# Performance work log

Measured on AMD Instinct MI355X. Metric: run time of the kernel, lower is better.

The kernel has to match this reference:

```python
import jax, jax.numpy as jnp
import numpy as np

B = 16        # batch
N = 1024      # satellite nodes
D = 256       # hidden size
H = 8         # attention heads
NUM_LAYERS = 3          # config.n_layer_aa
L = NUM_LAYERS + 1      # distinct GAT layers
EPS = 1e-5


def setup_inputs() -> dict:
    key = jax.random.key(0)
    ks = jax.random.split(key, 6)
    graph_vectors = jax.random.normal(ks[0], (B, N + 1, D), dtype=jnp.float32)
    graph = jax.random.uniform(ks[1], (B, N, N), dtype=jnp.float32)
    scale = 0.02
    Wq = jax.random.normal(ks[2], (L, D, D), dtype=jnp.float32) * scale
    Wk = jax.random.normal(ks[3], (L, D, D), dtype=jnp.float32) * scale
    Wv = jax.random.normal(ks[4], (L, D, D), dtype=jnp.float32) * scale
    Wo = jax.random.normal(ks[5], (L, D, D), dtype=jnp.float32) * scale
    ln_g = jnp.ones((L, D), dtype=jnp.float32)
    ln_b = jnp.zeros((L, D), dtype=jnp.float32)
    return {"graph_vectors": graph_vectors, "graph": graph,
            "Wq": Wq, "Wk": Wk, "Wv": Wv, "Wo": Wo,
            "ln_g": ln_g, "ln_b": ln_b}


def _layer_norm(x, g, b):
    mu = jnp.mean(x, axis=-1, keepdims=True)
    var = jnp.var(x, axis=-1, keepdims=True)
    return (x - mu) * jax.lax.rsqrt(var + EPS) * g + b


def _gat(x_q, x_kv, wq, wk, wv, wo, g, b):
    # multi-head attention: x_q [B,Lq,D] attends over x_kv [B,Lk,D]
    Bq, Lq, _ = x_q.shape
    Lk = x_kv.shape[1]
    dh = D // H
    q = (x_q @ wq).reshape(Bq, Lq, H, dh)
    k = (x_kv @ wk).reshape(Bq, Lk, H, dh)
    v = (x_kv @ wv).reshape(Bq, Lk, H, dh)
    scores = jnp.einsum('bqhd,bkhd->bhqk', q, k) / jnp.sqrt(jnp.float32(dh))
    attn = jax.nn.softmax(scores, axis=-1)
    o = jnp.einsum('bhqk,bkhd->bqhd', attn, v).reshape(Bq, Lq, D)
    out = o @ wo
    return _layer_norm(out + x_q, g, b)


def reference(graph_vectors, graph, Wq, Wk, Wv, Wo, ln_g, ln_b):
    relay = graph_vectors[:, :1, :]        # [B,1,D]
    sat = graph_vectors[:, 1:, :]          # [B,N,D]
    # layer 0: relay attends over satellites
    relay = _gat(relay, sat, Wq[0], Wk[0], Wv[0], Wo[0], ln_g[0], ln_b[0])
    # satellite = (satellite^T @ graph)^T -> [B,N,D]
    sat = jnp.einsum('bnd,bnm->bmd', sat, graph)
    gv = jnp.concatenate([relay, sat], axis=1)   # [B,N+1,D]
    # middle layers: full self-attention over all N+1 nodes
    for i in range(1, NUM_LAYERS):
        gv = _gat(gv, gv, Wq[i], Wk[i], Wv[i], Wo[i], ln_g[i], ln_b[i])
    relay_u = gv[:, :1, :]
    sat_u = gv[:, 1:, :]
    z = _gat(relay_u, sat_u, Wq[-1], Wk[-1], Wv[-1], Wo[-1], ln_g[-1], ln_b[-1])[:, 0, :]
    return z, sat_u
```

## Files before the change

kernel.cpp:

```cpp
#include <hip/hip_runtime.h>
#include <hip/hip_bf16.h>
#include <math.h>

#define BD   256
#define NH   8
#define DH   32
#define NB   16
#define NN   1024
#define LQ   1025
#define EPSV 1e-5f
#define KP   1088

typedef unsigned short ushort_t;
typedef __attribute__((ext_vector_type(8))) short short8;
typedef __attribute__((ext_vector_type(4))) float f32x4;

static __device__ __forceinline__ ushort_t f2b(float x) {
  union { __hip_bfloat16 h; ushort_t u; } cv;
  cv.h = __float2bfloat16(x);
  return cv.u;
}
static __device__ __forceinline__ float b2f(ushort_t u) {
  union { float f; unsigned v; } c; c.v = ((unsigned)u) << 16; return c.f;
}
static __device__ __forceinline__ float fexp2(float x) {
#if defined(__has_builtin)
#if __has_builtin(__builtin_amdgcn_exp2f)
  return __builtin_amdgcn_exp2f(x);
#else
  return exp2f(x);
#endif
#else
  return exp2f(x);
#endif
}

__global__ void k_copy_cast(const float* __restrict__ in, float* __restrict__ X,
                            ushort_t* __restrict__ Xh, long n) {
  long stride = (long)gridDim.x * 256;
  for (long i = (long)blockIdx.x * 256 + threadIdx.x; i < n; i += stride) {
    float v = in[i];
    X[i] = v;
    Xh[i] = f2b(v);
  }
}

__global__ void k_sat_out(const float* __restrict__ X, float* __restrict__ out) {
  long n = (long)NB * NN * BD;
  long stride = (long)gridDim.x * 256;
  for (long i = (long)blockIdx.x * 256 + threadIdx.x; i < n; i += stride) {
    long b = i / ((long)NN * BD);
    long r = i - b * ((long)NN * BD);
    out[i] = X[b * (long)LQ * BD + BD + r];
  }
}

__global__ __launch_bounds__(256) void k_wtrans(const float* __restrict__ Wq,
                                                const float* __restrict__ Wk,
                                                const float* __restrict__ Wv,
                                                const float* __restrict__ Wo,
                                                ushort_t* __restrict__ Wt) {
  const float C1 = 0.17677669529663687f * 1.4426950408889634f;
  int mat = blockIdx.y;
  int type = mat >> 2, layer = mat & 3;
  const float* src = (type == 0) ? Wq : (type == 1) ? Wk : (type == 2) ? Wv : Wo;
  src += (long)layer * BD * BD;
  float scv = (type == 0) ? C1 : 1.f;
  ushort_t* dst = Wt + (long)mat * BD * BD;
  __shared__ float t[32][33];
  int k0 = (blockIdx.x & 7) * 32, n0 = (blockIdx.x >> 3) * 32;
  int tid = threadIdx.x;
  for (int i = tid; i < 1024; i += 256) {
    int kk = i >> 5, nn = i & 31;
    t[kk][nn] = src[(long)(k0 + kk) * BD + n0 + nn];
  }
  __syncthreads();
  for (int i = tid; i < 1024; i += 256) {
    int nn = i >> 5, kk = i & 31;
    dst[(long)(n0 + nn) * BD + k0 + kk] = f2b(t[kk][nn] * scv);
  }
}

__global__ __launch_bounds__(256) void k_gtrans(const float* __restrict__ G,
                                                ushort_t* __restrict__ Ght) {
  __shared__ ushort_t t[64][65];
  int b = blockIdx.y;
  int m0 = (blockIdx.x & 15) * 64, n0 = (blockIdx.x >> 4) * 64;
  const float* Gb = G + (long)b * NN * NN;
  ushort_t* dst = Ght + (long)b * NN * NN;
  int tid = threadIdx.x;
  #pragma unroll
  for (int rr = 0; rr < 16; rr++) {
    int n = rr * 4 + (tid >> 6);
    int m = tid & 63;
    t[m][n] = f2b(Gb[(long)(n0 + n) * NN + m0 + m]);
  }
  __syncthreads();
  #pragma unroll
  for (int rr = 0; rr < 8; rr++) {
    int m = rr * 8 + (tid >> 5);
    int n2 = (tid & 31) * 2;
    unsigned w = (unsigned)t[m][n2] | ((unsigned)t[m][n2 + 1] << 16);
    *(unsigned*)&dst[(long)(m0 + m) * NN + n0 + n2] = w;
  }
}

__global__ __launch_bounds__(256) void k_satT(const ushort_t* __restrict__ Xh,
                                              ushort_t* __restrict__ satT) {
  __shared__ ushort_t t[64][65];
  int b = blockIdx.y;
  int n0 = (blockIdx.x & 15) * 64, d0 = (blockIdx.x >> 4) * 64;
  const ushort_t* src = Xh + ((long)b * LQ + 1) * BD;
  ushort_t* dst = satT + (long)b * BD * NN;
  int tid = threadIdx.x;
  #pragma unroll
  for (int rr = 0; rr < 16; rr++) {
    int n = rr * 4 + (tid >> 6);
    int d = tid & 63;
    t[n][d] = src[(long)(n0 + n) * BD + d0 + d];
  }
  __syncthreads();
  #pragma unroll
  for (int rr = 0; rr < 8; rr++) {
    int d = rr * 8 + (tid >> 5);
    int n2 = (tid & 31) * 2;
    unsigned w = (unsigned)t[n2][d] | ((unsigned)t[n2 + 1][d] << 16);
    *(unsigned*)&dst[(long)(d0 + d) * NN + n0 + n2] = w;
  }
}

__global__ __launch_bounds__(256) void k_vtrans(const ushort_t* __restrict__ Vh,
                                                ushort_t* __restrict__ VhT) {
  __shared__ ushort_t t[64][65];
  int b = blockIdx.z;
  int n0 = blockIdx.x * 64, d0 = blockIdx.y * 64;
  const ushort_t* src = Vh + (long)b * LQ * BD;
  ushort_t* dst = VhT + (long)b * BD * KP;
  int tid = threadIdx.x;
  #pragma unroll
  for (int rr = 0; rr < 16; rr++) {
    int n = rr * 4 + (tid >> 6);
    int d = tid & 63;
    int key = n0 + n;
    t[n][d] = (key < LQ) ? src[(long)key * BD + d0 + d] : (ushort_t)0;
  }
  __syncthreads();
  #pragma unroll
  for (int rr = 0; rr < 8; rr++) {
    int d = rr * 8 + (tid >> 5);
    int n2 = (tid & 31) * 2;
    unsigned w = (unsigned)t[n2][d] | ((unsigned)t[n2 + 1][d] << 16);
    *(unsigned*)&dst[(long)(d0 + d) * KP + n0 + n2] = w;
  }
}

static __device__ __forceinline__ void gemm_core(const ushort_t* __restrict__ A,
                                                 const ushort_t* __restrict__ W,
                                                 ushort_t* Ws,
                                                 float* __restrict__ Cf,
                                                 ushort_t* __restrict__ Ch,
                                                 int M, int m0, int n0) {
  int tid = threadIdx.x;
  int wave = tid >> 6, lane = tid & 63;
  int l15 = lane & 15, quad = lane >> 4;
  for (int i = tid; i < 64 * 32; i += 256) {
    int r = i >> 5, c8 = (i & 31) * 8;
    *(uint4*)&Ws[r * 264 + c8] = *(const uint4*)&W[(long)(n0 + r) * 256 + c8];
  }
  __syncthreads();
  int mrow = m0 + wave * 16 + l15;
  if (mrow > M - 1) mrow = M - 1;
  f32x4 acc[4];
  #pragma unroll
  for (int f = 0; f < 4; f++) { acc[f][0] = 0.f; acc[f][1] = 0.f; acc[f][2] = 0.f; acc[f][3] = 0.f; }
  #pragma unroll
  for (int k0 = 0; k0 < 256; k0 += 32) {
    short8 a = *(const short8*)&A[(long)mrow * 256 + k0 + quad * 8];
    #pragma unroll
    for (int f = 0; f < 4; f++) {
      short8 bb = *(const short8*)&Ws[(f * 16 + l15) * 264 + k0 + quad * 8];
      acc[f] = __builtin_amdgcn_mfma_f32_16x16x32_bf16(a, bb, acc[f], 0, 0, 0);
    }
  }
  #pragma unroll
  for (int f = 0; f < 4; f++)
    #pragma unroll
    for (int r = 0; r < 4; r++) {
      int m = m0 + wave * 16 + quad * 4 + r;
      if (m < M) {
        long idx = (long)m * 256 + n0 + f * 16 + l15;
        if (Cf) Cf[idx] = acc[f][r];
        else    Ch[idx] = f2b(acc[f][r]);
      }
    }
}

__global__ __launch_bounds__(256) void gemm_qkv(const ushort_t* __restrict__ Xh,
                                                const ushort_t* __restrict__ Wt, int layer,
                                                ushort_t* __restrict__ Qo,
                                                ushort_t* __restrict__ Ko,
                                                ushort_t* __restrict__ Vo, int M) {
  __shared__ __align__(16) ushort_t As[128 * 72];
  __shared__ __align__(16) ushort_t Bs[128 * 72];
  int tid = threadIdx.x;
  int wave = tid >> 6, lane = tid & 63;
  int l15 = lane & 15, quad = lane >> 4;
  int wr = wave >> 1, wc = wave & 1;
  int which = blockIdx.y >> 1;
  int n0 = (blockIdx.y & 1) * 128;
  const ushort_t* W = Wt + (long)(which * 4 + layer) * 65536;
  ushort_t* C = (which == 0) ? Qo : (which == 1) ? Ko : Vo;
  int m0 = blockIdx.x * 128;

  int sr = tid >> 2, sc = (tid & 3) * 8;
  int ar0 = m0 + sr;      if (ar0 > M - 1) ar0 = M - 1;
  int ar1 = m0 + sr + 64; if (ar1 > M - 1) ar1 = M - 1;
  const ushort_t* aSrc0 = Xh + (long)ar0 * 256 + sc;
  const ushort_t* aSrc1 = Xh + (long)ar1 * 256 + sc;
  const ushort_t* bSrc0 = W + (long)(n0 + sr) * 256 + sc;
  const ushort_t* bSrc1 = bSrc0 + 64 * 256;
  ushort_t* aDst0 = &As[sr * 72 + sc];
  ushort_t* aDst1 = aDst0 + 64 * 72;
  ushort_t* bDst0 = &Bs[sr * 72 + sc];
  ushort_t* bDst1 = bDst0 + 64 * 72;

  {
    uint4 a0 = *(const uint4*)aSrc0;
    uint4 a1 = *(const uint4*)aSrc1;
    uint4 b0 = *(const uint4*)bSrc0;
    uint4 b1 = *(const uint4*)bSrc1;
    *(uint4*)aDst0 = a0; *(uint4*)aDst1 = a1;
    *(uint4*)bDst0 = b0; *(uint4*)bDst1 = b1;
  }
  __syncthreads();

  f32x4 acc[4][4];
  #pragma unroll
  for (int i = 0; i < 4; i++)
    #pragma unroll
    for (int j = 0; j < 4; j++) { acc[i][j][0] = 0.f; acc[i][j][1] = 0.f; acc[i][j][2] = 0.f; acc[i][j][3] = 0.f; }

  for (int ks = 0; ks < 8; ks++) {
    bool more = (ks < 7);
    uint4 na0, na1, nb0, nb1;
    if (more) {
      aSrc0 += 32; aSrc1 += 32; bSrc0 += 32; bSrc1 += 32;
      na0 = *(const uint4*)aSrc0;
      na1 = *(const uint4*)aSrc1;
      nb0 = *(const uint4*)bSrc0;
      nb1 = *(const uint4*)bSrc1;
    }
    short8 af[4], bf[4];
    #pragma unroll
    for (int f = 0; f < 4; f++)
      af[f] = *(const short8*)&As[(wr * 64 + f * 16 + l15) * 72 + quad * 8];
    #pragma unroll
    for (int f = 0; f < 4; f++)
      bf[f] = *(const short8*)&Bs[(wc * 64 + f * 16 + l15) * 72 + quad * 8];
    #pragma unroll
    for (int i = 0; i < 4; i++)
      #pragma unroll
      for (int j = 0; j < 4; j++)
        acc[i][j] = __builtin_amdgcn_mfma_f32_16x16x32_bf16(af[i], bf[j], acc[i][j], 0, 0, 0);
    if (more) {
      __syncthreads();
      *(uint4*)aDst0 = na0;
      *(uint4*)aDst1 = na1;
      *(uint4*)bDst0 = nb0;
      *(uint4*)bDst1 = nb1;
      __syncthreads();
    }
  }

  #pragma unroll
  for (int i = 0; i < 4; i++)
    #pragma unroll
    for (int j = 0; j < 4; j++)
      #pragma unroll
      for (int r = 0; r < 4; r++) {
        int m = m0 + wr * 64 + i * 16 + quad * 4 + r;
        if (m < M) {
          int n = n0 + wc * 64 + j * 16 + l15;
          C[(long)m * 256 + n] = f2b(acc[i][j][r]);
        }
      }
}

__global__ __launch_bounds__(256) void gemm_kv(const ushort_t* __restrict__ Xh,
                                               const ushort_t* __restrict__ Wt, int layer,
                                               ushort_t* __restrict__ Ko,
                                               ushort_t* __restrict__ Vo) {
  __shared__ __align__(16) ushort_t Ws[64 * 264];
  int which = blockIdx.y >> 2, n0 = (blockIdx.y & 3) * 64;
  int b = blockIdx.z;
  const ushort_t* W = Wt + (long)((which + 1) * 4 + layer) * 65536;
  const ushort_t* A = Xh + (long)b * (LQ * BD) + BD;
  ushort_t* C = ((which == 0) ? Ko : Vo) + (long)b * (NN * BD);
  gemm_core(A, W, Ws, nullptr, C, NN, blockIdx.x * 64, n0);
}

__global__ __launch_bounds__(256) void gemm_oproj(const ushort_t* __restrict__ Oh,
                                                  const ushort_t* __restrict__ Wt, int layer,
                                                  float* __restrict__ Cf, int M) {
  __shared__ __align__(16) ushort_t Ws[64 * 264];
  gemm_core(Oh, Wt + (long)(12 + layer) * 65536, Ws, Cf, nullptr, M,
            blockIdx.x * 64, blockIdx.y * 64);
}

__global__ __launch_bounds__(256) void gemm_gtx2(const ushort_t* __restrict__ Ght,
                                                 const ushort_t* __restrict__ satT,
                                                 float* __restrict__ X,
                                                 ushort_t* __restrict__ Xh) {
  __shared__ __align__(16) ushort_t As[128 * 72];
  __shared__ __align__(16) ushort_t Bs[128 * 72];
  int b = blockIdx.z;
  const ushort_t* A  = Ght + (long)b * NN * NN;
  const ushort_t* Bp = satT + (long)b * BD * NN;
  int tid = threadIdx.x;
  int wave = tid >> 6, lane = tid & 63;
  int l15 = lane & 15, quad = lane >> 4;
  int wr = wave >> 1, wc = wave & 1;
  int m0 = blockIdx.x * 128, d0 = blockIdx.y * 128;

  int sr = tid >> 2, sc = (tid & 3) * 8;
  const ushort_t* aSrc0 = A  + (long)(m0 + sr) * NN + sc;
  const ushort_t* aSrc1 = aSrc0 + (long)64 * NN;
  const ushort_t* bSrc0 = Bp + (long)(d0 + sr) * NN + sc;
  const ushort_t* bSrc1 = bSrc0 + (long)64 * NN;
  ushort_t* aDst0 = &As[sr * 72 + sc];
  ushort_t* aDst1 = aDst0 + 64 * 72;
  ushort_t* bDst0 = &Bs[sr * 72 + sc];
  ushort_t* bDst1 = bDst0 + 64 * 72;

  {
    uint4 a0 = *(const uint4*)aSrc0;
    uint4 a1 = *(const uint4*)aSrc1;
    uint4 b0 = *(const uint4*)bSrc0;
    uint4 b1 = *(const uint4*)bSrc1;
    *(uint4*)aDst0 = a0; *(uint4*)aDst1 = a1;
    *(uint4*)bDst0 = b0; *(uint4*)bDst1 = b1;
  }
  __syncthreads();

  f32x4 acc[4][4];
  #pragma unroll
  for (int i = 0; i < 4; i++)
    #pragma unroll
    for (int j = 0; j < 4; j++) { acc[i][j][0] = 0.f; acc[i][j][1] = 0.f; acc[i][j][2] = 0.f; acc[i][j][3] = 0.f; }

  for (int ks = 0; ks < 32; ks++) {
    bool more = (ks < 31);
    uint4 na0, na1, nb0, nb1;
    if (more) {
      aSrc0 += 32; aSrc1 += 32; bSrc0 += 32; bSrc1 += 32;
      na0 = *(const uint4*)aSrc0;
      na1 = *(const uint4*)aSrc1;
      nb0 = *(const uint4*)bSrc0;
      nb1 = *(const uint4*)bSrc1;
    }
    short8 af[4], bf[4];
    #pragma unroll
    for (int f = 0; f < 4; f++)
      af[f] = *(const short8*)&As[(wr * 64 + f * 16 + l15) * 72 + quad * 8];
    #pragma unroll
    for (int f = 0; f < 4; f++)
      bf[f] = *(const short8*)&Bs[(wc * 64 + f * 16 + l15) * 72 + quad * 8];
    #pragma unroll
    for (int i = 0; i < 4; i++)
      #pragma unroll
      for (int j = 0; j < 4; j++)
        acc[i][j] = __builtin_amdgcn_mfma_f32_16x16x32_bf16(af[i], bf[j], acc[i][j], 0, 0, 0);
    if (more) {
      __syncthreads();
      *(uint4*)aDst0 = na0;
      *(uint4*)aDst1 = na1;
      *(uint4*)bDst0 = nb0;
      *(uint4*)bDst1 = nb1;
      __syncthreads();
    }
  }

  long xb = ((long)b * LQ + 1) * 256;
  #pragma unroll
  for (int i = 0; i < 4; i++)
    #pragma unroll
    for (int j = 0; j < 4; j++)
      #pragma unroll
      for (int r = 0; r < 4; r++) {
        int m = m0 + wr * 64 + i * 16 + quad * 4 + r;
        int d = d0 + wc * 64 + j * 16 + l15;
        long idx = xb + (long)m * 256 + d;
        X[idx] = acc[i][j][r];
        Xh[idx] = f2b(acc[i][j][r]);
      }
}

__global__ __launch_bounds__(256) void attn_fa(const ushort_t* __restrict__ Qh,
                                               const ushort_t* __restrict__ Kh,
                                               const ushort_t* __restrict__ VhT,
                                               ushort_t* __restrict__ Oh) {
  __shared__ __align__(16) ushort_t Ps[4][32][72];
  __shared__ __align__(16) ushort_t Kb[64 * 72];
  __shared__ __align__(16) ushort_t Vb[32 * 72];
  int tid = threadIdx.x;
  int wave = tid >> 6, lane = tid & 63;
  int l15 = lane & 15, quad = lane >> 4;
  int b = blockIdx.x >> 3, h = blockIdx.x & 7;
  long hb = ((long)b * LQ) * BD + h * DH;
  long vB = (long)b * BD * KP;
  int hd0 = h * DH;
  int q0 = blockIdx.y * 128 + wave * 32;
  int lq = lane & 48;

  short8 qB[2];
  #pragma unroll
  for (int t = 0; t < 2; t++) {
    int qc = q0 + t * 16 + l15; if (qc > LQ - 1) qc = LQ - 1;
    qB[t] = *(const short8*)&Qh[hb + (long)qc * BD + quad * 8];
  }

  short8 onesB;
  #pragma unroll
  for (int i = 0; i < 8; i++) onesB[i] = (short)0x3F80;

  const ushort_t *s0, *s1;
  ushort_t *d0, *d1;
  long stp;
  if (wave < 2) {
    int kt0 = wave * 2, kt1 = kt0 + 1;
    s0 = Kh + hb + (long)(kt0 * 16 + l15) * BD + quad * 8;
    s1 = Kh + hb + (long)(kt1 * 16 + l15) * BD + quad * 8;
    d0 = &Kb[(kt0 * 16 + l15) * 72 + quad * 8];
    d1 = &Kb[(kt1 * 16 + l15) * 72 + quad * 8];
    stp = (long)64 * BD;
  } else {
    int sa = (wave - 2) * 2, sb = sa + 1;
    s0 = VhT + vB + (long)(hd0 + (sa >> 1) * 16 + l15) * KP + (sa & 1) * 32 + quad * 8;
    s1 = VhT + vB + (long)(hd0 + (sb >> 1) * 16 + l15) * KP + (sb & 1) * 32 + quad * 8;
    d0 = &Vb[((sa >> 1) * 16 + l15) * 72 + (sa & 1) * 32 + quad * 8];
    d1 = &Vb[((sb >> 1) * 16 + l15) * 72 + (sb & 1) * 32 + quad * 8];
    stp = 64;
  }
  {
    uint4 r0 = *(const uint4*)s0;
    uint4 r1 = *(const uint4*)s1;
    *(uint4*)d0 = r0;
    *(uint4*)d1 = r1;
  }
  __syncthreads();

  f32x4 o[2][2];
  #pragma unroll
  for (int t = 0; t < 2; t++)
    #pragma unroll
    for (int dt = 0; dt < 2; dt++) { o[t][dt][0] = 0.f; o[t][dt][1] = 0.f; o[t][dt][2] = 0.f; o[t][dt][3] = 0.f; }
  f32x4 lsa[2];
  lsa[0][0] = 0.f; lsa[0][1] = 0.f; lsa[0][2] = 0.f; lsa[0][3] = 0.f;
  lsa[1][0] = 0.f; lsa[1][1] = 0.f; lsa[1][2] = 0.f; lsa[1][3] = 0.f;
  float m[2] = {-1e30f, -1e30f};
  f32x4 zf; zf[0] = 0.f; zf[1] = 0.f; zf[2] = 0.f; zf[3] = 0.f;

  for (int c = 0; c < 17; c++) {
    bool more = (c < 16);
    uint4 n0, n1;
    if (more) {
      if (c == 15 && wave < 2) {
        const ushort_t* cl = Kh + hb + (long)(LQ - 1) * BD + quad * 8;
        n0 = *(const uint4*)cl;
        n1 = n0;
      } else {
        s0 += stp; s1 += stp;
        n0 = *(const uint4*)s0;
        n1 = *(const uint4*)s1;
      }
    }
    short8 ka[4];
    #pragma unroll
    for (int kt = 0; kt < 4; kt++)
      ka[kt] = *(const short8*)&Kb[(kt * 16 + l15) * 72 + quad * 8];

    bool tail = (c == 16);
    #pragma unroll
    for (int t = 0; t < 2; t++) {
      f32x4 s[4];
      #pragma unroll
      for (int kt = 0; kt < 4; kt++)
        s[kt] = __builtin_amdgcn_mfma_f32_16x16x32_bf16(ka[kt], qB[t], zf, 0, 0, 0);
      if (tail) {
        #pragma unroll
        for (int kt = 0; kt < 4; kt++)
          #pragma unroll
          for (int r = 0; r < 4; r++)
            if (kt + r) s[kt][r] = -1e30f;
        if (quad) s[0][0] = -1e30f;
      }
      float cm = fmaxf(fmaxf(s[0][0], s[0][1]), fmaxf(s[0][2], s[0][3]));
      cm = fmaxf(cm, fmaxf(fmaxf(s[1][0], s[1][1]), fmaxf(s[1][2], s[1][3])));
      cm = fmaxf(cm, fmaxf(fmaxf(s[2][0], s[2][1]), fmaxf(s[2][2], s[2][3])));
      cm = fmaxf(cm, fmaxf(fmaxf(s[3][0], s[3][1]), fmaxf(s[3][2], s[3][3])));
      cm = fmaxf(cm, __shfl_xor(cm, 16));
      cm = fmaxf(cm, __shfl_xor(cm, 32));
      if (__any(cm > m[t] + 8.f)) {
        float mn = fmaxf(m[t], cm);
        float f = fexp2(m[t] - mn);
        m[t] = mn;
        #pragma unroll
        for (int r = 0; r < 4; r++) {
          float fr = __shfl(f, lq | (quad * 4 + r));
          o[t][0][r] *= fr;
          o[t][1][r] *= fr;
          lsa[t][r] *= fr;
        }
      }
      float mt = m[t];
      #pragma unroll
      for (int kt = 0; kt < 4; kt++) {
        float p0 = fexp2(s[kt][0] - mt);
        float p1 = fexp2(s[kt][1] - mt);
        float p2 = fexp2(s[kt][2] - mt);
        float p3 = fexp2(s[kt][3] - mt);
        unsigned lo = (unsigned)f2b(p0) | ((unsigned)f2b(p1) << 16);
        unsigned hi = (unsigned)f2b(p2) | ((unsigned)f2b(p3) << 16);
        uint2 w; w.x = lo; w.y = hi;
        *(uint2*)&Ps[wave][t * 16 + l15][kt * 16 + quad * 4] = w;
      }
    }
    short8 vb[2][2];
    #pragma unroll
    for (int dt = 0; dt < 2; dt++)
      #pragma unroll
      for (int ks = 0; ks < 2; ks++)
        vb[ks][dt] = *(const short8*)&Vb[(dt * 16 + l15) * 72 + ks * 32 + quad * 8];
    #pragma unroll
    for (int ks = 0; ks < 2; ks++) {
      short8 pa0 = *(const short8*)&Ps[wave][l15][ks * 32 + quad * 8];
      short8 pa1 = *(const short8*)&Ps[wave][16 + l15][ks * 32 + quad * 8];
      lsa[0] = __builtin_amdgcn_mfma_f32_16x16x32_bf16(pa0, onesB, lsa[0], 0, 0, 0);
      lsa[1] = __builtin_amdgcn_mfma_f32_16x16x32_bf16(pa1, onesB, lsa[1], 0, 0, 0);
      #pragma unroll
      for (int dt = 0; dt < 2; dt++) {
        o[0][dt] = __builtin_amdgcn_mfma_f32_16x16x32_bf16(pa0, vb[ks][dt], o[0][dt], 0, 0, 0);
        o[1][dt] = __builtin_amdgcn_mfma_f32_16x16x32_bf16(pa1, vb[ks][dt], o[1][dt], 0, 0, 0);
      }
    }
    if (more) {
      __syncthreads();
      *(uint4*)d0 = n0;
      *(uint4*)d1 = n1;
      __syncthreads();
    }
  }
  #pragma unroll
  for (int mt = 0; mt < 2; mt++) {
    #pragma unroll
    for (int r = 0; r < 4; r++) {
      int row = q0 + mt * 16 + quad * 4 + r;
      if (row < LQ) {
        float den = lsa[mt][r];
        float inv = (den > 0.f) ? 1.f / den : 0.f;
        #pragma unroll
        for (int dt = 0; dt < 2; dt++)
          Oh[hb + (long)row * BD + dt * 16 + l15] = f2b(o[mt][dt][r] * inv);
      }
    }
  }
}

__global__ __launch_bounds__(256) void attn_relay(const float* __restrict__ q,
                                                  const ushort_t* __restrict__ K,
                                                  const ushort_t* __restrict__ V,
                                                  float* __restrict__ o) {
  int b = blockIdx.x, h = blockIdx.y;
  int tid = threadIdx.x;
  const float scale = 0.17677669529663687f;
  __shared__ float s[NN];
  __shared__ float qs[DH];
  __shared__ float rbuf[256];
  __shared__ float part[8][33];
  if (tid < DH) qs[tid] = q[(long)b * BD + h * DH + tid];
  __syncthreads();
  long base = ((long)b * NN) * BD + h * DH;
  for (int k = tid; k < NN; k += 256) {
    float dot = 0.f;
    const ushort_t* kr = &K[base + (long)k * BD];
    #pragma unroll
    for (int d2 = 0; d2 < 16; d2++) {
      unsigned w = *(const unsigned*)&kr[d2 * 2];
      dot += qs[d2 * 2] * b2f((ushort_t)(w & 0xffff)) + qs[d2 * 2 + 1] * b2f((ushort_t)(w >> 16));
    }
    s[k] = dot * scale;
  }
  __syncthreads();
  float m = -1e30f;
  for (int k = tid; k < NN; k += 256) m = fmaxf(m, s[k]);
  rbuf[tid] = m;
  __syncthreads();
  for (int st = 128; st > 0; st >>= 1) {
    if (tid < st) rbuf[tid] = fmaxf(rbuf[tid], rbuf[tid + st]);
    __syncthreads();
  }
  float mx = rbuf[0];
  __syncthreads();
  float sm = 0.f;
  for (int k = tid; k < NN; k += 256) {
    float p = __expf(s[k] - mx);
    s[k] = p;
    sm += p;
  }
  rbuf[tid] = sm;
  __syncthreads();
  for (int st = 128; st > 0; st >>= 1) {
    if (tid < st) rbuf[tid] += rbuf[tid + st];
    __syncthreads();
  }
  float inv = 1.f / rbuf[0];
  int d = tid & 31, slice = tid >> 5;
  float acc = 0.f;
  for (int k = slice; k < NN; k += 8) acc += s[k] * b2f(V[base + (long)k * BD + d]);
  part[slice][d] = acc;
  __syncthreads();
  if (tid < DH) {
    float ss = 0.f;
    #pragma unroll
    for (int t = 0; t < 8; t++) ss += part[t][tid];
    o[(long)b * BD + h * DH + tid] = ss * inv;
  }
}

__global__ __launch_bounds__(256) void rowvec_matmul(const float* __restrict__ X, long xstride,
                                                     const float* __restrict__ W,
                                                     float* __restrict__ out) {
  int b = blockIdx.x, tid = threadIdx.x;
  __shared__ float xs[BD];
  xs[tid] = X[(long)b * xstride + tid];
  __syncthreads();
  float acc = 0.f;
  for (int k = 0; k < BD; k++) acc += xs[k] * W[(long)k * BD + tid];
  out[(long)b * BD + tid] = acc;
}

__global__ __launch_bounds__(256) void rowvec_oproj_ln(const float* __restrict__ o,
                                                       const float* __restrict__ Wo,
                                                       const float* __restrict__ Xres, long xstride,
                                                       const float* __restrict__ g,
                                                       const float* __restrict__ beta,
                                                       float* __restrict__ dst, long dstride,
                                                       ushort_t* __restrict__ dsth, long dhstride) {
  int b = blockIdx.x, tid = threadIdx.x;
  __shared__ float xs[BD];
  __shared__ float rs[256], rq[256];
  xs[tid] = o[(long)b * BD + tid];
  __syncthreads();
  float acc = 0.f;
  for (int k = 0; k < BD; k++) acc += xs[k] * Wo[(long)k * BD + tid];
  float v = acc + Xres[(long)b * xstride + tid];
  rs[tid] = v;
  rq[tid] = v * v;
  __syncthreads();
  for (int st = 128; st > 0; st >>= 1) {
    if (tid < st) { rs[tid] += rs[tid + st]; rq[tid] += rq[tid + st]; }
    __syncthreads();
  }
  float mu = rs[0] * (1.f / BD);
  float var = rq[0] * (1.f / BD) - mu * mu;
  float y = (v - mu) * rsqrtf(var + EPSV) * g[tid] + beta[tid];
  dst[(long)b * dstride + tid] = y;
  if (dsth) dsth[(long)b * dhstride + tid] = f2b(y);
}

__global__ __launch_bounds__(256) void ln_residual(const float* __restrict__ OP,
                                                   float* __restrict__ X,
                                                   ushort_t* __restrict__ Xh,
                                                   const float* __restrict__ g,
                                                   const float* __restrict__ beta) {
  long r = blockIdx.x;
  int tid = threadIdx.x;
  __shared__ float rs[256], rq[256];
  float v = OP[r * BD + tid] + X[r * BD + tid];
  rs[tid] = v;
  rq[tid] = v * v;
  __syncthreads();
  for (int st = 128; st > 0; st >>= 1) {
    if (tid < st) { rs[tid] += rs[tid + st]; rq[tid] += rq[tid + st]; }
    __syncthreads();
  }
  float mu = rs[0] * (1.f / BD);
  float var = rq[0] * (1.f / BD) - mu * mu;
  float y = (v - mu) * rsqrtf(var + EPSV) * g[tid] + beta[tid];
  X[r * BD + tid] = y;
  Xh[r * BD + tid] = f2b(y);
}

extern "C" void kernel_launch(void* const* d_in, const int* in_sizes, int n_in,
                              void* d_out, int out_size, void* d_ws, size_t ws_size,
                              hipStream_t stream) {
  const float* gv    = (const float*)d_in[0];
  const float* graph = (const float*)d_in[1];
  const float* Wq    = (const float*)d_in[2];
  const float* Wk    = (const float*)d_in[3];
  const float* Wv    = (const float*)d_in[4];
  const float* Wo    = (const float*)d_in[5];
  const float* lg    = (const float*)d_in[6];
  const float* lb    = (const float*)d_in[7];
  float* out = (float*)d_out;

  const long S  = (long)NB * LQ * BD;
  const long S4 = S * 4, S2 = S * 2;
  char* base = (char*)d_ws;
  float*    X    = (float*)base;
  ushort_t* Xh   = (ushort_t*)(base + S4);
  float*    B1   = (float*)(base + S4 + S2);
  ushort_t* Qh   = (ushort_t*)(base + 2 * S4 + S2);
  ushort_t* Kh   = (ushort_t*)(base + 2 * S4 + 2 * S2);
  ushort_t* Vh   = (ushort_t*)(base + 2 * S4 + 3 * S2);
  ushort_t* Oh   = (ushort_t*)(base + 2 * S4 + 4 * S2);
  ushort_t* Wt   = (ushort_t*)(base + 2 * S4 + 5 * S2);
  float*    qrel = (float*)(base + 2 * S4 + 5 * S2 + 16L * 65536 * 2);
  float*    orel = qrel + (long)NB * BD;
  ushort_t* Ght  = (ushort_t*)B1;
  ushort_t* satT = Vh;
  ushort_t* VhT  = (ushort_t*)B1;

  const long WSZ = (long)BD * BD;
  const long XST = (long)LQ * BD;
  dim3 blk(256);

  k_copy_cast<<<dim3(2048), blk, 0, stream>>>(gv, X, Xh, S);
  k_wtrans<<<dim3(64, 16), blk, 0, stream>>>(Wq, Wk, Wv, Wo, Wt);

  rowvec_matmul<<<dim3(NB), blk, 0, stream>>>(X, XST, Wq + 0 * WSZ, qrel);
  gemm_kv<<<dim3(16, 8, NB), blk, 0, stream>>>(Xh, Wt, 0, Kh, Vh);
  attn_relay<<<dim3(NB, NH), blk, 0, stream>>>(qrel, Kh, Vh, orel);
  rowvec_oproj_ln<<<dim3(NB), blk, 0, stream>>>(orel, Wo + 0 * WSZ, X, XST,
                                                lg + 0 * BD, lb + 0 * BD, X, XST, Xh, XST);

  k_gtrans<<<dim3(256, NB), blk, 0, stream>>>(graph, Ght);
  k_satT<<<dim3(64, NB), blk, 0, stream>>>(Xh, satT);
  gemm_gtx2<<<dim3(8, 2, NB), blk, 0, stream>>>(Ght, satT, X, Xh);

  for (int l = 1; l <= 2; l++) {
    gemm_qkv<<<dim3(129, 6), blk, 0, stream>>>(Xh, Wt, l, Qh, Kh, Vh, NB * LQ);
    k_vtrans<<<dim3(17, 4, NB), blk, 0, stream>>>(Vh, VhT);
    attn_fa<<<dim3(NB * NH, 9), blk, 0, stream>>>(Qh, Kh, VhT, Oh);
    gemm_oproj<<<dim3(257, 4), blk, 0, stream>>>(Oh, Wt, l, B1, NB * LQ);
    ln_residual<<<dim3(NB * LQ), blk, 0, stream>>>(B1, X, Xh, lg + l * BD, lb + l * BD);
  }

  k_sat_out<<<dim3(2048), blk, 0, stream>>>(X, out + (long)NB * BD);

  rowvec_matmul<<<dim3(NB), blk, 0, stream>>>(X, XST, Wq + 3 * WSZ, qrel);
  gemm_kv<<<dim3(16, 8, NB), blk, 0, stream>>>(Xh, Wt, 3, Kh, Vh);
  attn_relay<<<dim3(NB, NH), blk, 0, stream>>>(qrel, Kh, Vh, orel);
  rowvec_oproj_ln<<<dim3(NB), blk, 0, stream>>>(orel, Wo + 3 * WSZ, X, XST,
                                                lg + 3 * BD, lb + 3 * BD, out, BD, nullptr, 0);
}
```

Before: 541.3 us.

## Share 128x128 GEMM core for kv/oproj; compute attention row sums with scalar adds

```diff
diff --git a/kernel.cpp b/kernel.cpp
--- a/kernel.cpp
+++ b/kernel.cpp
@@ -154,69 +154,22 @@
   }
 }
 
-static __device__ __forceinline__ void gemm_core(const ushort_t* __restrict__ A,
-                                                 const ushort_t* __restrict__ W,
-                                                 ushort_t* Ws,
-                                                 float* __restrict__ Cf,
-                                                 ushort_t* __restrict__ Ch,
-                                                 int M, int m0, int n0) {
-  int tid = threadIdx.x;
-  int wave = tid >> 6, lane = tid & 63;
-  int l15 = lane & 15, quad = lane >> 4;
-  for (int i = tid; i < 64 * 32; i += 256) {
-    int r = i >> 5, c8 = (i & 31) * 8;
-    *(uint4*)&Ws[r * 264 + c8] = *(const uint4*)&W[(long)(n0 + r) * 256 + c8];
-  }
-  __syncthreads();
-  int mrow = m0 + wave * 16 + l15;
-  if (mrow > M - 1) mrow = M - 1;
-  f32x4 acc[4];
-  #pragma unroll
-  for (int f = 0; f < 4; f++) { acc[f][0] = 0.f; acc[f][1] = 0.f; acc[f][2] = 0.f; acc[f][3] = 0.f; }
-  #pragma unroll
-  for (int k0 = 0; k0 < 256; k0 += 32) {
-    short8 a = *(const short8*)&A[(long)mrow * 256 + k0 + quad * 8];
-    #pragma unroll
-    for (int f = 0; f < 4; f++) {
-      short8 bb = *(const short8*)&Ws[(f * 16 + l15) * 264 + k0 + quad * 8];
-      acc[f] = __builtin_amdgcn_mfma_f32_16x16x32_bf16(a, bb, acc[f], 0, 0, 0);
-    }
-  }
-  #pragma unroll
-  for (int f = 0; f < 4; f++)
-    #pragma unroll
-    for (int r = 0; r < 4; r++) {
-      int m = m0 + wave * 16 + quad * 4 + r;
-      if (m < M) {
-        long idx = (long)m * 256 + n0 + f * 16 + l15;
-        if (Cf) Cf[idx] = acc[f][r];
-        else    Ch[idx] = f2b(acc[f][r]);
-      }
-    }
-}
-
-__global__ __launch_bounds__(256) void gemm_qkv(const ushort_t* __restrict__ Xh,
-                                                const ushort_t* __restrict__ Wt, int layer,
-                                                ushort_t* __restrict__ Qo,
-                                                ushort_t* __restrict__ Ko,
-                                                ushort_t* __restrict__ Vo, int M) {
-  __shared__ __align__(16) ushort_t As[128 * 72];
-  __shared__ __align__(16) ushort_t Bs[128 * 72];
+static __device__ __forceinline__ void core128(const ushort_t* __restrict__ A,
+                                               const ushort_t* __restrict__ W,
+                                               ushort_t* As, ushort_t* Bs,
+                                               int M, int m0, int n0,
+                                               float* __restrict__ Cf,
+                                               ushort_t* __restrict__ Ch) {
   int tid = threadIdx.x;
   int wave = tid >> 6, lane = tid & 63;
   int l15 = lane & 15, quad = lane >> 4;
   int wr = wave >> 1, wc = wave & 1;
-  int which = blockIdx.y >> 1;
-  int n0 = (blockIdx.y & 1) * 128;
-  const ushort_t* W = Wt + (long)(which * 4 + layer) * 65536;
-  ushort_t* C = (which == 0) ? Qo : (which == 1) ? Ko : Vo;
-  int m0 = blockIdx.x * 128;
 
   int sr = tid >> 2, sc = (tid & 3) * 8;
   int ar0 = m0 + sr;      if (ar0 > M - 1) ar0 = M - 1;
   int ar1 = m0 + sr + 64; if (ar1 > M - 1) ar1 = M - 1;
-  const ushort_t* aSrc0 = Xh + (long)ar0 * 256 + sc;
-  const ushort_t* aSrc1 = Xh + (long)ar1 * 256 + sc;
+  const ushort_t* aSrc0 = A + (long)ar0 * 256 + sc;
+  const ushort_t* aSrc1 = A + (long)ar1 * 256 + sc;
   const ushort_t* bSrc0 = W + (long)(n0 + sr) * 256 + sc;
   const ushort_t* bSrc1 = bSrc0 + 64 * 256;
   ushort_t* aDst0 = &As[sr * 72 + sc];
@@ -280,31 +233,49 @@
       for (int r = 0; r < 4; r++) {
         int m = m0 + wr * 64 + i * 16 + quad * 4 + r;
         if (m < M) {
-          int n = n0 + wc * 64 + j * 16 + l15;
-          C[(long)m * 256 + n] = f2b(acc[i][j][r]);
+          long idx = (long)m * 256 + n0 + wc * 64 + j * 16 + l15;
+          if (Cf) Cf[idx] = acc[i][j][r];
+          else    Ch[idx] = f2b(acc[i][j][r]);
         }
       }
+}
+
+__global__ __launch_bounds__(256) void gemm_qkv(const ushort_t* __restrict__ Xh,
+                                                const ushort_t* __restrict__ Wt, int layer,
+                                                ushort_t* __restrict__ Qo,
+                                                ushort_t* __restrict__ Ko,
+                                                ushort_t* __restrict__ Vo, int M) {
+  __shared__ __align__(16) ushort_t As[128 * 72];
+  __shared__ __align__(16) ushort_t Bs[128 * 72];
+  int which = blockIdx.y >> 1;
+  int n0 = (blockIdx.y & 1) * 128;
+  const ushort_t* W = Wt + (long)(which * 4 + layer) * 65536;
+  ushort_t* C = (which == 0) ? Qo : (which == 1) ? Ko : Vo;
+  core128(Xh, W, As, Bs, M, blockIdx.x * 128, n0, nullptr, C);
 }
 
 __global__ __launch_bounds__(256) void gemm_kv(const ushort_t* __restrict__ Xh,
                                                const ushort_t* __restrict__ Wt, int layer,
                                                ushort_t* __restrict__ Ko,
                                                ushort_t* __restrict__ Vo) {
-  __shared__ __align__(16) ushort_t Ws[64 * 264];
-  int which = blockIdx.y >> 2, n0 = (blockIdx.y & 3) * 64;
+  __shared__ __align__(16) ushort_t As[128 * 72];
+  __shared__ __align__(16) ushort_t Bs[128 * 72];
+  int which = blockIdx.y >> 1;
+  int n0 = (blockIdx.y & 1) * 128;
   int b = blockIdx.z;
   const ushort_t* W = Wt + (long)((which + 1) * 4 + layer) * 65536;
   const ushort_t* A = Xh + (long)b * (LQ * BD) + BD;
   ushort_t* C = ((which == 0) ? Ko : Vo) + (long)b * (NN * BD);
-  gemm_core(A, W, Ws, nullptr, C, NN, blockIdx.x * 64, n0);
+  core128(A, W, As, Bs, NN, blockIdx.x * 128, n0, nullptr, C);
 }
 
 __global__ __launch_bounds__(256) void gemm_oproj(const ushort_t* __restrict__ Oh,
                                                   const ushort_t* __restrict__ Wt, int layer,
                                                   float* __restrict__ Cf, int M) {
-  __shared__ __align__(16) ushort_t Ws[64 * 264];
-  gemm_core(Oh, Wt + (long)(12 + layer) * 65536, Ws, Cf, nullptr, M,
-            blockIdx.x * 64, blockIdx.y * 64);
+  __shared__ __align__(16) ushort_t As[128 * 72];
+  __shared__ __align__(16) ushort_t Bs[128 * 72];
+  core128(Oh, Wt + (long)(12 + layer) * 65536, As, Bs, M,
+          blockIdx.x * 128, blockIdx.y * 128, Cf, nullptr);
 }
 
 __global__ __launch_bounds__(256) void gemm_gtx2(const ushort_t* __restrict__ Ght,
@@ -402,6 +373,7 @@
   __shared__ __align__(16) ushort_t Ps[4][32][72];
   __shared__ __align__(16) ushort_t Kb[64 * 72];
   __shared__ __align__(16) ushort_t Vb[32 * 72];
+  __shared__ float Lbuf[4][32];
   int tid = threadIdx.x;
   int wave = tid >> 6, lane = tid & 63;
   int l15 = lane & 15, quad = lane >> 4;
@@ -418,10 +390,6 @@
     int qc = q0 + t * 16 + l15; if (qc > LQ - 1) qc = LQ - 1;
     qB[t] = *(const short8*)&Qh[hb + (long)qc * BD + quad * 8];
   }
-
-  short8 onesB;
-  #pragma unroll
-  for (int i = 0; i < 8; i++) onesB[i] = (short)0x3F80;
 
   const ushort_t *s0, *s1;
   ushort_t *d0, *d1;
@@ -454,10 +422,8 @@
   for (int t = 0; t < 2; t++)
     #pragma unroll
     for (int dt = 0; dt < 2; dt++) { o[t][dt][0] = 0.f; o[t][dt][1] = 0.f; o[t][dt][2] = 0.f; o[t][dt][3] = 0.f; }
-  f32x4 lsa[2];
-  lsa[0][0] = 0.f; lsa[0][1] = 0.f; lsa[0][2] = 0.f; lsa[0][3] = 0.f;
-  lsa[1][0] = 0.f; lsa[1][1] = 0.f; lsa[1][2] = 0.f; lsa[1][3] = 0.f;
   float m[2] = {-1e30f, -1e30f};
+  float ls[2] = {0.f, 0.f};
   f32x4 zf; zf[0] = 0.f; zf[1] = 0.f; zf[2] = 0.f; zf[3] = 0.f;
 
   for (int c = 0; c < 17; c++) {
@@ -503,13 +469,13 @@
       if (__any(cm > m[t] + 8.f)) {
         float mn = fmaxf(m[t], cm);
         float f = fexp2(m[t] - mn);
+        ls[t] *= f;
         m[t] = mn;
         #pragma unroll
         for (int r = 0; r < 4; r++) {
           float fr = __shfl(f, lq | (quad * 4 + r));
           o[t][0][r] *= fr;
           o[t][1][r] *= fr;
-          lsa[t][r] *= fr;
         }
       }
       float mt = m[t];
@@ -519,6 +485,7 @@
         float p1 = fexp2(s[kt][1] - mt);
         float p2 = fexp2(s[kt][2] - mt);
         float p3 = fexp2(s[kt][3] - mt);
+        ls[t] += (p0 + p1) + (p2 + p3);
         unsigned lo = (unsigned)f2b(p0) | ((unsigned)f2b(p1) << 16);
         unsigned hi = (unsigned)f2b(p2) | ((unsigned)f2b(p3) << 16);
         uint2 w; w.x = lo; w.y = hi;
@@ -535,8 +502,6 @@
     for (int ks = 0; ks < 2; ks++) {
       short8 pa0 = *(const short8*)&Ps[wave][l15][ks * 32 + quad * 8];
       short8 pa1 = *(const short8*)&Ps[wave][16 + l15][ks * 32 + quad * 8];
-      lsa[0] = __builtin_amdgcn_mfma_f32_16x16x32_bf16(pa0, onesB, lsa[0], 0, 0, 0);
-      lsa[1] = __builtin_amdgcn_mfma_f32_16x16x32_bf16(pa1, onesB, lsa[1], 0, 0, 0);
       #pragma unroll
       for (int dt = 0; dt < 2; dt++) {
         o[0][dt] = __builtin_amdgcn_mfma_f32_16x16x32_bf16(pa0, vb[ks][dt], o[0][dt], 0, 0, 0);
@@ -551,12 +516,23 @@
     }
   }
   #pragma unroll
+  for (int t = 0; t < 2; t++) {
+    ls[t] += __shfl_xor(ls[t], 16);
+    ls[t] += __shfl_xor(ls[t], 32);
+  }
+  if (quad == 0) {
+    Lbuf[wave][l15] = ls[0];
+    Lbuf[wave][16 + l15] = ls[1];
+  }
+  __syncthreads();
+  #pragma unroll
   for (int mt = 0; mt < 2; mt++) {
+    f32x4 lv = *(const f32x4*)&Lbuf[wave][mt * 16 + quad * 4];
     #pragma unroll
     for (int r = 0; r < 4; r++) {
       int row = q0 + mt * 16 + quad * 4 + r;
       if (row < LQ) {
-        float den = lsa[mt][r];
+        float den = lv[r];
         float inv = (den > 0.f) ? 1.f / den : 0.f;
         #pragma unroll
         for (int dt = 0; dt < 2; dt++)
@@ -729,7 +705,7 @@
   k_wtrans<<<dim3(64, 16), blk, 0, stream>>>(Wq, Wk, Wv, Wo, Wt);
 
   rowvec_matmul<<<dim3(NB), blk, 0, stream>>>(X, XST, Wq + 0 * WSZ, qrel);
-  gemm_kv<<<dim3(16, 8, NB), blk, 0, stream>>>(Xh, Wt, 0, Kh, Vh);
+  gemm_kv<<<dim3(8, 4, NB), blk, 0, stream>>>(Xh, Wt, 0, Kh, Vh);
   attn_relay<<<dim3(NB, NH), blk, 0, stream>>>(qrel, Kh, Vh, orel);
   rowvec_oproj_ln<<<dim3(NB), blk, 0, stream>>>(orel, Wo + 0 * WSZ, X, XST,
                                                 lg + 0 * BD, lb + 0 * BD, X, XST, Xh, XST);
@@ -742,14 +718,14 @@
     gemm_qkv<<<dim3(129, 6), blk, 0, stream>>>(Xh, Wt, l, Qh, Kh, Vh, NB * LQ);
     k_vtrans<<<dim3(17, 4, NB), blk, 0, stream>>>(Vh, VhT);
     attn_fa<<<dim3(NB * NH, 9), blk, 0, stream>>>(Qh, Kh, VhT, Oh);
-    gemm_oproj<<<dim3(257, 4), blk, 0, stream>>>(Oh, Wt, l, B1, NB * LQ);
+    gemm_oproj<<<dim3(129, 2), blk, 0, stream>>>(Oh, Wt, l, B1, NB * LQ);
     ln_residual<<<dim3(NB * LQ), blk, 0, stream>>>(B1, X, Xh, lg + l * BD, lb + l * BD);
   }
 
   k_sat_out<<<dim3(2048), blk, 0, stream>>>(X, out + (long)NB * BD);
 
   rowvec_matmul<<<dim3(NB), blk, 0, stream>>>(X, XST, Wq + 3 * WSZ, qrel);
-  gemm_kv<<<dim3(16, 8, NB), blk, 0, stream>>>(Xh, Wt, 3, Kh, Vh);
+  gemm_kv<<<dim3(8, 4, NB), blk, 0, stream>>>(Xh, Wt, 3, Kh, Vh);
   attn_relay<<<dim3(NB, NH), blk, 0, stream>>>(qrel, Kh, Vh, orel);
   rowvec_oproj_ln<<<dim3(NB), blk, 0, stream>>>(orel, Wo + 3 * WSZ, X, XST,
                                                 lg + 3 * BD, lb + 3 * BD, out, BD, nullptr, 0);
```

Result: no change. 531.1 us (-1.9%).
